# Kernel optimization log

Measured on AMD Instinct MI355X. Metric: run time of the kernel, lower is better.

Reference implementation:

```python
import jax, jax.numpy as jnp
import numpy as np

TOPK = 16          # static stand-in for dense_to_sparse(A_virtual): top-k neighbors per master node
LAMBDA_ATTN = 1.0  # VirtualGeneration temperature
GAMMA = 4.0        # gaussian radial basis width
R_CENTERS = 8      # radial_embedding.out_dim
NEG = -1e9


def _sh(v):
    # stand-in spherical harmonics: 16 monomials (lmax=3-ish) of the unit direction
    n = jnp.linalg.norm(v, axis=-1, keepdims=True)
    u = v / (n + 1e-9)
    x, y, z = u[:, 0], u[:, 1], u[:, 2]
    o = jnp.ones_like(x)
    return jnp.stack([o, x, y, z, x * x, y * y, z * z, x * y, x * z, y * z,
                      x * x * x, y * y * y, z * z * z, x * x * y, y * y * z, z * z * x], axis=-1)


def _radial(r):
    # gaussian radial basis, r: [E,1] -> [E,R]
    centers = jnp.linspace(0.0, 5.0, R_CENTERS, dtype=r.dtype)
    return jnp.exp(-GAMMA * (r - centers[None, :]) ** 2)


def _msgs(x, src, dst, sh, feats, Wr, wsh, n):
    # MACE-style conv message aggregation: radial-gated, SH-modulated gather/scatter
    gate = feats @ Wr                               # [E, Cin]
    msg = x[src] * gate * (sh @ wsh)[:, None]       # [E, Cin]
    return jax.ops.segment_sum(msg, dst, num_segments=n)


def _forward(h, pos, edge_index, edge_sh, edge_feats,
             W_loc_r, w_loc_sh, W_loc_out, W_prod_loc,
             W_ms1, b_ms1, W_ms2, b_ms2, Wq, Wk,
             W_a1, b_a1, W_a2, b_a2,
             W_h_r, w_h_sh, W_h_out, W_prod_h):
    N, D = h.shape
    D2 = W_loc_out.shape[1]
    S = W_ms1.shape[0]
    src, dst = edge_index[0], edge_index[1]

    # --- local conv + prod skip (h_local) ---
    h_up = _msgs(h, src, dst, edge_sh, edge_feats, W_loc_r, w_loc_sh, N) @ W_loc_out  # [N, D2]
    h_local = h_up @ W_prod_loc + jnp.pad(h, ((0, 0), (0, D2 - D)))
    h_scalar = h_local[:, :S]

    # --- master selection (MLP -> sigmoid -> hard threshold) ---
    m = jax.nn.sigmoid(jax.nn.relu(h_scalar @ W_ms1 + b_ms1) @ W_ms2 + b_ms2)[:, 0]
    mf = (m > 0.5).astype(h.dtype)

    # --- induced master-master edges: mask instead of dynamic subgraph extraction ---
    pair = mf[src] * mf[dst]
    vec_i = pos[src] - pos[dst]
    len_i = jnp.linalg.norm(vec_i, axis=-1, keepdims=True)
    sh_i = _sh(vec_i)
    rf_i = _radial(len_i) * pair[:, None]  # induced full_weights == 1, masked to master pairs

    # --- virtual edge generation: dense attention scores among masters, static top-k ---
    q = h_scalar @ Wq
    kk = h_scalar @ Wk
    scores_nn = (q @ kk.T) / (np.sqrt(S).astype(np.float32) * LAMBDA_ATTN)  # [N, N]
    pair_ok = (mf[:, None] * mf[None, :]) * (1.0 - jnp.eye(N, dtype=h.dtype))  # no self loops
    scores_nn = jnp.where(pair_ok > 0, scores_nn, NEG)
    topv, topi = jax.lax.top_k(scores_nn, TOPK)        # [N, K]
    vsrc = jnp.repeat(jnp.arange(N), TOPK)             # [N*K]
    vdst = topi.reshape(-1)
    vvalid = (topv.reshape(-1) > NEG / 2).astype(h.dtype)

    vec_v = pos[vsrc] - pos[vdst]
    len_v = jnp.linalg.norm(vec_v, axis=-1, keepdims=True)
    sh_v = _sh(vec_v)
    rf_v = _radial(len_v)

    # --- scatter-softmax attention over virtual edges (per destination) ---
    attn_in = jnp.concatenate([h_scalar[vsrc], h_scalar[vdst], rf_v], axis=-1)
    sc = (jax.nn.relu(attn_in @ W_a1 + b_a1) @ W_a2 + b_a2)[:, 0]
    sc = jnp.where(vvalid > 0, sc, NEG)
    mx = jax.ops.segment_max(sc, vdst, num_segments=N)
    ex = jnp.where(vvalid > 0, jnp.exp(sc - mx[vdst]), 0.0)
    den = jax.ops.segment_sum(ex, vdst, num_segments=N)
    wv = ex / (den[vdst] + 1e-12)
    rf_v = rf_v * wv[:, None]

    # --- hierarchical conv over induced + virtual master edges ---
    agg = (_msgs(h_local, src, dst, sh_i, rf_i, W_h_r, w_h_sh, N)
           + _msgs(h_local, vsrc, vdst, sh_v, rf_v, W_h_r, w_h_sh, N))
    h_m_up = agg @ W_h_out
    h_hier = (h_m_up @ W_prod_h + h_local) * mf[:, None]  # zero at non-master slots

    # --- gated combine ---
    return (1.0 - m)[:, None] * h_local + m[:, None] * h_hier


def setup_inputs():
    key = jax.random.key(0)
    ks = jax.random.split(key, 24)
    N, E, D, D2, S, R, L, HID = 4096, 131072, 128, 256, 128, 8, 16, 64

    def w(k, shape):
        return (jax.random.normal(k, shape, jnp.float32) / np.sqrt(shape[0]).astype(np.float32))

    return dict(
        h=jax.random.normal(ks[0], (N, D), jnp.float32),
        pos=jax.random.normal(ks[1], (N, 3), jnp.float32),
        edge_index=jax.random.randint(ks[2], (2, E), 0, N),
        edge_sh=jax.random.normal(ks[3], (E, L), jnp.float32),
        edge_feats=jax.random.normal(ks[4], (E, R), jnp.float32),
        batch=jnp.zeros((N,), jnp.int32),
        W_loc_r=w(ks[5], (R, D)),
        w_loc_sh=jax.random.normal(ks[6], (L,), jnp.float32) / 4.0,
        W_loc_out=w(ks[7], (D, D2)),
        W_prod_loc=w(ks[8], (D2, D2)),
        W_ms1=w(ks[9], (S, HID)), b_ms1=jnp.zeros((HID,), jnp.float32),
        W_ms2=w(ks[10], (HID, 1)), b_ms2=jnp.zeros((1,), jnp.float32),
        Wq=w(ks[11], (S, S)), Wk=w(ks[12], (S, S)),
        W_a1=w(ks[13], (2 * S + R, S)), b_a1=jnp.zeros((S,), jnp.float32),
        W_a2=w(ks[14], (S, 1)), b_a2=jnp.zeros((1,), jnp.float32),
        W_h_r=w(ks[15], (R, D2)),
        w_h_sh=jax.random.normal(ks[16], (L,), jnp.float32) / 4.0,
        W_h_out=w(ks[17], (D2, D2)),
        W_prod_h=w(ks[18], (D2, D2)),
    )


def reference(h, pos, edge_index, edge_sh, edge_feats, batch,
              W_loc_r, w_loc_sh, W_loc_out, W_prod_loc,
              W_ms1, b_ms1, W_ms2, b_ms2, Wq, Wk,
              W_a1, b_a1, W_a2, b_a2,
              W_h_r, w_h_sh, W_h_out, W_prod_h):
    # batch is unused by the original forward as well
    return _forward(h, pos, edge_index, edge_sh, edge_feats,
                    W_loc_r, w_loc_sh, W_loc_out, W_prod_loc,
                    W_ms1, b_ms1, W_ms2, b_ms2, Wq, Wk,
                    W_a1, b_a1, W_a2, b_a2,
                    W_h_r, w_h_sh, W_h_out, W_prod_h)
```

## Files before the change

kernel.cpp:

```cpp
#include <hip/hip_runtime.h>

typedef unsigned int u32;

#define NN 4096
#define EE 131072
#define DD 128
#define D2 256
#define SS 128
#define RR 8
#define LL 16
#define HH 64
#define TK 16
#define VSTRIDE 32
#define VV2 (NN*VSTRIDE)
#define NEGF -1000000000.0f
#define MNEGF -3.0e38f
#define SCLF 11.313708305358886719f
#define DELTA 1.0e-3f
#define CHUNK 1024
#define RCH 32
#define VCH 64
#define MAXCH_R 8192
#define MAXCH_V 5184

__device__ __forceinline__ float fadd(float a, float b) { return __fadd_rn(a, b); }
__device__ __forceinline__ float fsub(float a, float b) { return __fsub_rn(a, b); }
__device__ __forceinline__ float fmul(float a, float b) { return __fmul_rn(a, b); }
__device__ __forceinline__ float ffma(float a, float b, float c) { return __fmaf_rn(a, b, c); }

enum : size_t {
  B_CNTR   = 0,
  B_CNTV   = 16384,
  B_MXE    = 32768,
  ZERO_END = 49152,
  B_STARTR = 49152,
  B_STARTV = 69632,
  B_LISTR  = 90112,
  B_LISTV  = 614400,
  B_TOPI   = 1138688,
  B_WFAC   = 1662976,
  B_AMSG   = 2187264,
  B_HUP    = 4284416,
  B_HLOC   = 8478720,
  B_T1     = 12673024,
  B_MARR   = 13721600,
  B_MF     = 13737984,
  B_Q      = 13754368,
  B_KT     = 15851520,
  B_SC     = 17948672,
  B_WV     = 18472960,
  B_SUMR   = 18997248,
  B_SUMV   = 23191552,
  B_AGG    = 27385856,
  B_HMUP   = 31580160,
  B_CURR   = 35774464,
  B_CURV   = 35790848,
  B_P1     = 35807232,
  B_P2     = 37904384,
  B_TOTAL  = 40001536,
  B_ERP    = B_Q,
  B_EVP    = B_HUP,
  B_SHV1   = B_SUMR,
  B_SCHUNK = B_SUMR,
  B_CHT    = B_HUP + 3145728,
  O_CHJV   = 64,
  O_CHPV   = 64 + 4*MAXCH_V,
  O_CHJR   = 64 + 8*MAXCH_V,
  O_CHPR   = 64 + 8*MAXCH_V + 4*MAXCH_R,
  B_CHT2   = 40001536,
  B_SBIG   = 41943040,
  WS_BIG   = 109051904
};

__global__ void count_keys(const int* __restrict__ keys, int n, u32* __restrict__ cnt) {
  int e = blockIdx.x * 256 + threadIdx.x;
  if (e >= n) return;
  int d = keys[e];
  if (d >= 0) atomicAdd(&cnt[d], 1u);
}

__global__ __launch_bounds__(256) void scan_ex_par(const u32* __restrict__ cnt,
                                                   u32* __restrict__ start,
                                                   u32* __restrict__ cursor, int n,
                                                   int csz, u32* __restrict__ chCnt,
                                                   int* __restrict__ chJ,
                                                   int* __restrict__ chP) {
  __shared__ u32 part[256];
  __shared__ u32 cpart[256];
  int t = threadIdx.x;
  int per = n / 256;
  u32 s = 0;
  for (int i = 0; i < per; ++i) s += cnt[t*per + i];
  part[t] = s;
  __syncthreads();
  if (t == 0) {
    u32 run = 0;
    for (int i = 0; i < 256; ++i) { u32 v = part[i]; part[i] = run; run += v; }
    start[n] = run;
  }
  __syncthreads();
  u32 run = part[t];
  for (int i = 0; i < per; ++i) {
    int k = t*per + i;
    start[k] = run;
    cursor[k] = run;
    run += cnt[k];
  }
  if (csz > 0) {
    u32 cc = 0;
    for (int i = 0; i < per; ++i) {
      u32 len = cnt[t*per + i];
      cc += (len + (u32)csz - 1u) / (u32)csz;
    }
    cpart[t] = cc;
    __syncthreads();
    if (t == 0) {
      u32 r2 = 0;
      for (int i = 0; i < 256; ++i) { u32 v = cpart[i]; cpart[i] = r2; r2 += v; }
      *chCnt = r2;
    }
    __syncthreads();
    u32 b = cpart[t];
    u32 sb = part[t];
    for (int i = 0; i < per; ++i) {
      int k = t*per + i;
      u32 len = cnt[k];
      u32 nch = (len + (u32)csz - 1u) / (u32)csz;
      for (u32 kk = 0; kk < nch; ++kk) { chJ[b] = k; chP[b] = (int)(sb + kk*(u32)csz); ++b; }
      sb += len;
    }
  }
}

__global__ void fill_atomic(const int* __restrict__ keys, int n,
                            u32* __restrict__ cursor, int* __restrict__ list) {
  int e = blockIdx.x * 256 + threadIdx.x;
  if (e >= n) return;
  int d = keys[e];
  if (d < 0) return;
  u32 p = atomicAdd(&cursor[d], 1u);
  list[p] = e;
}

__global__ void build_chunks(const u32* __restrict__ start, int nseg, int csz,
                             u32* __restrict__ cnt, int* __restrict__ chJ,
                             int* __restrict__ chP) {
  int j = blockIdx.x * 256 + threadIdx.x;
  if (j >= nseg) return;
  u32 s0 = start[j], s1 = start[j + 1];
  if (s0 >= s1) return;
  int nch = (int)((s1 - s0) + (u32)csz - 1) / csz;
  u32 b = atomicAdd(cnt, (u32)nch);
  for (int k = 0; k < nch; ++k) {
    chJ[b + k] = j;
    chP[b + k] = (int)(s0 + (u32)k * (u32)csz);
  }
}

__global__ void edge_pre1(const float* __restrict__ esh, const float* __restrict__ wsh,
                          float* __restrict__ shv1) {
  int e = blockIdx.x * 256 + threadIdx.x;
  if (e >= EE) return;
  float s = 0.f;
  #pragma unroll
  for (int l = 0; l < LL; ++l) s = ffma(esh[e*LL + l], wsh[l], s);
  shv1[e] = s;
}

__global__ __launch_bounds__(128) void rep_msgs1(
    const float* __restrict__ h, const int* __restrict__ ei,
    const float* __restrict__ efeat,
    const float* __restrict__ Wr, const float* __restrict__ shv1,
    const u32* __restrict__ startR, const int* __restrict__ listR,
    float* __restrict__ amsg)
{
  __shared__ int   ssrc[64];
  __shared__ float sshv[64];
  __shared__ float sef[64][8];
  int d = blockIdx.x, c = threadIdx.x;
  float wr[RR];
  #pragma unroll
  for (int r = 0; r < RR; ++r) wr[r] = Wr[r*DD + c];
  float acc = 0.f;
  u32 s0 = startR[d], s1 = startR[d + 1];
  for (u32 t0 = s0; t0 < s1; t0 += 64) {
    int tl = (int)(s1 - t0 < 64u ? s1 - t0 : 64u);
    if (c < tl) {
      int e = listR[t0 + c];
      ssrc[c] = ei[e];
      sshv[c] = shv1[e];
      const float4* fe = reinterpret_cast<const float4*>(&efeat[(size_t)e*RR]);
      float4 f0 = fe[0], f1 = fe[1];
      sef[c][0]=f0.x; sef[c][1]=f0.y; sef[c][2]=f0.z; sef[c][3]=f0.w;
      sef[c][4]=f1.x; sef[c][5]=f1.y; sef[c][6]=f1.z; sef[c][7]=f1.w;
    }
    __syncthreads();
    int k = 0;
    for (; k + 4 <= tl; k += 4) {
      float h0 = h[(size_t)ssrc[k  ]*DD + c];
      float h1 = h[(size_t)ssrc[k+1]*DD + c];
      float h2 = h[(size_t)ssrc[k+2]*DD + c];
      float h3 = h[(size_t)ssrc[k+3]*DD + c];
      float g0 = 0.f, g1 = 0.f, g2 = 0.f, g3 = 0.f;
      #pragma unroll
      for (int r = 0; r < RR; ++r) {
        g0 = ffma(sef[k  ][r], wr[r], g0);
        g1 = ffma(sef[k+1][r], wr[r], g1);
        g2 = ffma(sef[k+2][r], wr[r], g2);
        g3 = ffma(sef[k+3][r], wr[r], g3);
      }
      acc = fadd(acc, fmul(fmul(h0, g0), sshv[k  ]));
      acc = fadd(acc, fmul(fmul(h1, g1), sshv[k+1]));
      acc = fadd(acc, fmul(fmul(h2, g2), sshv[k+2]));
      acc = fadd(acc, fmul(fmul(h3, g3), sshv[k+3]));
    }
    for (; k < tl; ++k) {
      float hv = h[(size_t)ssrc[k]*DD + c];
      float g = 0.f;
      #pragma unroll
      for (int r = 0; r < RR; ++r) g = ffma(sef[k][r], wr[r], g);
      acc = fadd(acc, fmul(fmul(hv, g), sshv[k]));
    }
    __syncthreads();
  }
  amsg[d*DD + c] = acc;
}

__global__ __launch_bounds__(256) void gemm64(
    const float* __restrict__ A, int lda,
    const float* __restrict__ B, int ldb,
    float* __restrict__ C, int ldc,
    int K, int mode,
    const float* __restrict__ x1,
    const float* __restrict__ marr, const float* __restrict__ mfarr,
    float* __restrict__ outp)
{
  __shared__ float As[16][68];
  __shared__ float Bs[16][68];
  int tid = threadIdx.x;
  int bm = blockIdx.x << 6, bn = blockIdx.y << 6;
  int tm = ((tid >> 4) << 2), tn = ((tid & 15) << 2);
  float acc[4][4] = {};
  for (int k0 = 0; k0 < K; k0 += 16) {
    #pragma unroll
    for (int t = 0; t < 4; ++t) {
      int idx = tid + (t << 8);
      int r = idx >> 4, c = idx & 15;
      As[c][r] = A[(size_t)(bm + r)*lda + k0 + c];
      int rb = idx >> 6, cb = idx & 63;
      Bs[rb][cb] = B[(size_t)(k0 + rb)*ldb + bn + cb];
    }
    __syncthreads();
    #pragma unroll
    for (int kk = 0; kk < 16; ++kk) {
      float4 av = *reinterpret_cast<const float4*>(&As[kk][tm]);
      float4 bv = *reinterpret_cast<const float4*>(&Bs[kk][tn]);
      float a0 = av.x, a1 = av.y, a2 = av.z, a3 = av.w;
      float b0 = bv.x, b1 = bv.y, b2 = bv.z, b3 = bv.w;
      acc[0][0]=ffma(a0,b0,acc[0][0]); acc[0][1]=ffma(a0,b1,acc[0][1]);
      acc[0][2]=ffma(a0,b2,acc[0][2]); acc[0][3]=ffma(a0,b3,acc[0][3]);
      acc[1][0]=ffma(a1,b0,acc[1][0]); acc[1][1]=ffma(a1,b1,acc[1][1]);
      acc[1][2]=ffma(a1,b2,acc[1][2]); acc[1][3]=ffma(a1,b3,acc[1][3]);
      acc[2][0]=ffma(a2,b0,acc[2][0]); acc[2][1]=ffma(a2,b1,acc[2][1]);
      acc[2][2]=ffma(a2,b2,acc[2][2]); acc[2][3]=ffma(a2,b3,acc[2][3]);
      acc[3][0]=ffma(a3,b0,acc[3][0]); acc[3][1]=ffma(a3,b1,acc[3][1]);
      acc[3][2]=ffma(a3,b2,acc[3][2]); acc[3][3]=ffma(a3,b3,acc[3][3]);
    }
    __syncthreads();
  }
  #pragma unroll
  for (int ii = 0; ii < 4; ++ii) {
    int r = bm + tm + ii;
    #pragma unroll
    for (int jj = 0; jj < 4; ++jj) {
      int c = bn + tn + jj;
      float v = acc[ii][jj];
      if (mode == 0) {
        C[(size_t)r*ldc + c] = v;
      } else if (mode == 1) {
        if (c < DD) v = fadd(v, x1[(size_t)r*DD + c]);
        C[(size_t)r*ldc + c] = v;
      } else if (mode == 2) {
        float hl = x1[(size_t)r*D2 + c];
        float hh = fmul(fadd(v, hl), mfarr[r]);
        float m = marr[r];
        outp[(size_t)r*D2 + c] = fadd(fmul(fsub(1.f, m), hl), fmul(m, hh));
      } else {
        C[(size_t)c*ldc + r] = v;
      }
    }
  }
}

__global__ __launch_bounds__(256, 2) void gemm_score128(
    const float* __restrict__ A, const float* __restrict__ B,
    const float* __restrict__ mf, int rowoff,
    float* __restrict__ S)
{
  __shared__ float As[16][68];
  __shared__ float Bs[16][136];
  int tid = threadIdx.x;
  int bm = blockIdx.x << 6;
  int bn = blockIdx.y << 7;
  int tm = ((tid >> 4) << 2), tn = ((tid & 15) << 2);
  float acc[4][8] = {};
  for (int k0 = 0; k0 < SS; k0 += 16) {
    {
      int row = tid >> 2, seg = tid & 3;
      const float4 av = *reinterpret_cast<const float4*>(
          &A[(size_t)(bm + row)*SS + k0 + (seg << 2)]);
      As[(seg<<2)+0][row] = av.x;
      As[(seg<<2)+1][row] = av.y;
      As[(seg<<2)+2][row] = av.z;
      As[(seg<<2)+3][row] = av.w;
    }
    #pragma unroll
    for (int t = 0; t < 2; ++t) {
      int f = tid + (t << 8);
      int rb = f >> 5, cb = (f & 31) << 2;
      const float4 bv = *reinterpret_cast<const float4*>(
          &B[(size_t)(k0 + rb)*NN + bn + cb]);
      *reinterpret_cast<float4*>(&Bs[rb][cb]) = bv;
    }
    __syncthreads();
    #pragma unroll
    for (int kk = 0; kk < 16; ++kk) {
      float4 av = *reinterpret_cast<const float4*>(&As[kk][tm]);
      float4 bl = *reinterpret_cast<const float4*>(&Bs[kk][tn]);
      float4 bh = *reinterpret_cast<const float4*>(&Bs[kk][tn + 64]);
      float a[4] = {av.x, av.y, av.z, av.w};
      float b[8] = {bl.x, bl.y, bl.z, bl.w, bh.x, bh.y, bh.z, bh.w};
      #pragma unroll
      for (int i = 0; i < 4; ++i)
        #pragma unroll
        for (int j = 0; j < 8; ++j)
          acc[i][j] = ffma(a[i], b[j], acc[i][j]);
    }
    __syncthreads();
  }
  #pragma unroll
  for (int ii = 0; ii < 4; ++ii) {
    int r = bm + tm + ii;
    int rg = rowoff + r;
    #pragma unroll
    for (int jj = 0; jj < 8; ++jj) {
      int c = bn + ((jj < 4) ? (tn + jj) : (tn + 64 + (jj - 4)));
      float s = __fdiv_rn(acc[ii][jj], SCLF);
      bool valid = (mf[c] > 0.5f) && (c != rg);
      S[(size_t)r*NN + c] = valid ? s : NEGF;
    }
  }
}

__global__ __launch_bounds__(256) void rep_sel(
    const float* __restrict__ S, int rowoff, const float* __restrict__ mf,
    int* __restrict__ topi, float* __restrict__ wfac)
{
  __shared__ float svals[4];
  __shared__ int   sidx[4];
  int tid = threadIdx.x;
  int row = rowoff + blockIdx.x;
  int base = row * VSTRIDE;
  if (mf[row] <= 0.5f) {
    if (tid < VSTRIDE) { topi[base + tid] = -1; wfac[base + tid] = 0.f; }
    return;
  }
  float4 vals[4];
  const float4* rp = reinterpret_cast<const float4*>(S + (size_t)blockIdx.x * NN);
  #pragma unroll
  for (int g = 0; g < 4; ++g) vals[g] = rp[tid + (g << 8)];
  int w = tid >> 6, lane = tid & 63;
  float v15 = 0.f, v16 = 0.f; int i15 = -1, i16 = -1;
  for (int it = 0; it < 17; ++it) {
    float bv = MNEGF; int bi = 1 << 30;
    #pragma unroll
    for (int g = 0; g < 4; ++g) {
      int j0 = (tid << 2) + (g << 10);
      { float v = vals[g].x; int j = j0;     if (v > bv || (v == bv && j < bi)) { bv = v; bi = j; } }
      { float v = vals[g].y; int j = j0 + 1; if (v > bv || (v == bv && j < bi)) { bv = v; bi = j; } }
      { float v = vals[g].z; int j = j0 + 2; if (v > bv || (v == bv && j < bi)) { bv = v; bi = j; } }
      { float v = vals[g].w; int j = j0 + 3; if (v > bv || (v == bv && j < bi)) { bv = v; bi = j; } }
    }
    #pragma unroll
    for (int off = 32; off > 0; off >>= 1) {
      float v2 = __shfl_down(bv, off);
      int j2 = __shfl_down(bi, off);
      if (v2 > bv || (v2 == bv && j2 < bi)) { bv = v2; bi = j2; }
    }
    if (lane == 0) { svals[w] = bv; sidx[w] = bi; }
    __syncthreads();
    float fv = svals[0]; int fi = sidx[0];
    #pragma unroll
    for (int k = 1; k < 4; ++k) {
      float v2 = svals[k]; int j2 = sidx[k];
      if (v2 > fv || (v2 == fv && j2 < fi)) { fv = v2; fi = j2; }
    }
    __syncthreads();
    #pragma unroll
    for (int g = 0; g < 4; ++g) {
      int j0 = (tid << 2) + (g << 10);
      if (fi == j0)     vals[g].x = MNEGF;
      if (fi == j0 + 1) vals[g].y = MNEGF;
      if (fi == j0 + 2) vals[g].z = MNEGF;
      if (fi == j0 + 3) vals[g].w = MNEGF;
    }
    if (it < 15) {
      if (tid == 0) {
        bool ok = fv > 0.5f * NEGF;
        topi[base + it] = ok ? fi : -1;
        wfac[base + it] = ok ? 1.f : 0.f;
      }
    } else if (it == 15) { v15 = fv; i15 = fi; }
    else                 { v16 = fv; i16 = fi; }
  }
  if (tid == 0) {
    bool b16 = v15 > 0.5f * NEGF;
    bool b17 = v16 > 0.5f * NEGF;
    bool contested = b16 && b17 && (fsub(v15, v16) < DELTA);
    topi[base + 15] = b16 ? i15 : -1;
    wfac[base + 15] = b16 ? (contested ? 0.5f : 1.f) : 0.f;
    topi[base + 16] = contested ? i16 : -1;
    wfac[base + 16] = contested ? 0.5f : 0.f;
  }
  if (tid >= 17 && tid < VSTRIDE) { topi[base + tid] = -1; wfac[base + tid] = 0.f; }
}

__global__ __launch_bounds__(64) void rep_mask(const float* __restrict__ t1,
    const float* __restrict__ b1, const float* __restrict__ W2,
    const float* __restrict__ b2, float* __restrict__ marr, float* __restrict__ mf)
{
  __shared__ float t3[HH];
  int n = blockIdx.x, hh = threadIdx.x;
  t3[hh] = fmaxf(fadd(t1[n*HH + hh], b1[hh]), 0.f);
  __syncthreads();
  if (hh == 0) {
    float acc = 0.f;
    for (int k = 0; k < HH; ++k) acc = ffma(t3[k], W2[k], acc);
    float z = fadd(acc, b2[0]);
    float m = __fdiv_rn(1.f, fadd(1.f, expf(-z)));
    marr[n] = m;
    mf[n] = (m > 0.5f) ? 1.f : 0.f;
  }
}

__device__ __forceinline__ float centerf(int r) {
  return (float)(((double)r * 5.0) / 7.0);
}

__global__ __launch_bounds__(256) void attn_edge2(
    const float* __restrict__ P1, const float* __restrict__ P2,
    const float* __restrict__ pos, const int* __restrict__ topi,
    const float* __restrict__ Wa1, const float* __restrict__ ba1,
    const float* __restrict__ Wa2, const float* __restrict__ ba2,
    float* __restrict__ sc, u32* __restrict__ mxe)
{
  __shared__ float wsum[4];
  __shared__ float srf[2][8];
  int tid = threadIdx.x;
  int eh = tid >> 7;
  int c = tid & 127;
  int idx = blockIdx.x * 2 + eh;
  int i = idx / 17;
  int k = idx - i * 17;
  int v = (i << 5) + k;
  int j = topi[v];
  if (c < 8 && j >= 0) {
    float vx = fsub(pos[i*3+0], pos[j*3+0]);
    float vy = fsub(pos[i*3+1], pos[j*3+1]);
    float vz = fsub(pos[i*3+2], pos[j*3+2]);
    float n2 = fadd(fadd(fmul(vx,vx), fmul(vy,vy)), fmul(vz,vz));
    float len = __fsqrt_rn(n2);
    float dr = fsub(len, centerf(c));
    srf[eh][c] = expf(fmul(-4.f, fmul(dr, dr)));
  }
  __syncthreads();
  float p = 0.f;
  if (j >= 0) {
    float t = fadd(P1[(size_t)i*SS + c], P2[(size_t)j*SS + c]);
    #pragma unroll
    for (int r = 0; r < RR; ++r) {
      t = ffma(srf[eh][r], Wa1[(256 + r)*SS + c], t);
    }
    t = fmaxf(fadd(t, ba1[c]), 0.f);
    p = fmul(t, Wa2[c]);
  }
  #pragma unroll
  for (int off = 32; off > 0; off >>= 1) p += __shfl_down(p, off);
  int wid = tid >> 6;
  if ((tid & 63) == 0) wsum[wid] = p;
  __syncthreads();
  if ((tid & 127) == 0 && j >= 0) {
    float acc = wsum[eh*2] + wsum[eh*2 + 1];
    float s = fadd(acc, ba2[0]);
    sc[v] = s;
    u32 u = __float_as_uint(s);
    u = (u & 0x80000000u) ? ~u : (u | 0x80000000u);
    atomicMax(&mxe[j], u);
  }
}

__global__ __launch_bounds__(64) void rep_denwv2(
    const float* __restrict__ sc, const u32* __restrict__ mxe,
    const u32* __restrict__ startV, const int* __restrict__ listV,
    const float* __restrict__ wfac, float* __restrict__ wvv)
{
  int j = blockIdx.x;
  int lane = threadIdx.x;
  u32 s0 = startV[j], s1 = startV[j + 1];
  if (s0 == s1) return;
  u32 ue = mxe[j];
  u32 b = (ue & 0x80000000u) ? (ue ^ 0x80000000u) : ~ue;
  float mx = __uint_as_float(b);
  float psum = 0.f;
  for (u32 idx = s0 + lane; idx < s1; idx += 64) {
    int v = listV[idx];
    float ex = fmul(wfac[v], expf(fsub(sc[v], mx)));
    wvv[v] = ex;
    psum += ex;
  }
  #pragma unroll
  for (int off = 32; off > 0; off >>= 1) psum += __shfl_down(psum, off);
  float den = __shfl(psum, 0);
  float dd = fadd(den, 1e-12f);
  for (u32 idx = s0 + lane; idx < s1; idx += 64) {
    int v = listV[idx];
    wvv[v] = __fdiv_rn(wvv[v], dd);
  }
}

__device__ __forceinline__ float shrep(float vx, float vy, float vz,
                                       const float* __restrict__ w) {
  float n2 = fadd(fadd(fmul(vx,vx), fmul(vy,vy)), fmul(vz,vz));
  float n = __fsqrt_rn(n2);
  float dnm = fadd(n, 1e-9f);
  float x = __fdiv_rn(vx, dnm), y = __fdiv_rn(vy, dnm), z = __fdiv_rn(vz, dnm);
  float t[16];
  t[0]=1.f; t[1]=x; t[2]=y; t[3]=z;
  t[4]=fmul(x,x); t[5]=fmul(y,y); t[6]=fmul(z,z);
  t[7]=fmul(x,y); t[8]=fmul(x,z); t[9]=fmul(y,z);
  t[10]=fmul(fmul(x,x),x); t[11]=fmul(fmul(y,y),y); t[12]=fmul(fmul(z,z),z);
  t[13]=fmul(fmul(x,x),y); t[14]=fmul(fmul(y,y),z); t[15]=fmul(fmul(z,z),x);
  float s = 0.f;
  #pragma unroll
  for (int l = 0; l < 16; ++l) s = ffma(t[l], w[l], s);
  return s;
}

__global__ void edge_pre_rv(const float* __restrict__ pos, const int* __restrict__ ei,
                            const float* __restrict__ mf, const float* __restrict__ whsh,
                            const int* __restrict__ listR, float* __restrict__ erp,
                            const int* __restrict__ topi, const float* __restrict__ wvv,
                            const u32* __restrict__ startV, const int* __restrict__ listV,
                            float* __restrict__ evp) {
  int b = blockIdx.x;
  if (b < EE/256) {
    int p = b * 256 + threadIdx.x;
    int e = listR[p];
    int src = ei[e], dst = ei[EE + e];
    float* op = erp + (size_t)p * 9;
    if (mf[src] <= 0.5f || mf[dst] <= 0.5f) {
      #pragma unroll
      for (int r = 0; r < 9; ++r) op[r] = 0.f;
      return;
    }
    float vx = fsub(pos[src*3+0], pos[dst*3+0]);
    float vy = fsub(pos[src*3+1], pos[dst*3+1]);
    float vz = fsub(pos[src*3+2], pos[dst*3+2]);
    op[0] = shrep(vx, vy, vz, whsh);
    float len = __fsqrt_rn(fadd(fadd(fmul(vx,vx), fmul(vy,vy)), fmul(vz,vz)));
    #pragma unroll
    for (int r = 0; r < RR; ++r) {
      float dr = fsub(len, centerf(r));
      op[1 + r] = expf(fmul(-4.f, fmul(dr, dr)));
    }
  } else {
    int p = (b - EE/256) * 256 + threadIdx.x;
    if (p >= (int)startV[NN]) return;
    int v = listV[p];
    int i = v >> 5;
    int j = topi[v];
    float w = wvv[v];
    float* op = evp + (size_t)p * 9;
    float vx = fsub(pos[i*3+0], pos[j*3+0]);
    float vy = fsub(pos[i*3+1], pos[j*3+1]);
    float vz = fsub(pos[i*3+2], pos[j*3+2]);
    op[0] = shrep(vx, vy, vz, whsh);
    float len = __fsqrt_rn(fadd(fadd(fmul(vx,vx), fmul(vy,vy)), fmul(vz,vz)));
    #pragma unroll
    for (int r = 0; r < RR; ++r) {
      float dr = fsub(len, centerf(r));
      op[1 + r] = fmul(expf(fmul(-4.f, fmul(dr, dr))), w);
    }
  }
}

__global__ __launch_bounds__(256) void rep_msgs2r4(
    const float* __restrict__ hloc, const int* __restrict__ ei,
    const float* __restrict__ Whr, const float* __restrict__ erp,
    const u32* __restrict__ startR, const int* __restrict__ listR,
    const u32* __restrict__ cnt, const int* __restrict__ chJ,
    const int* __restrict__ chP, float* __restrict__ sumR)
{
  __shared__ int   ssrc[RCH];
  __shared__ float sep[RCH][9];
  int b = blockIdx.x;
  if (b >= (int)(*cnt)) return;
  int d = chJ[b], c = threadIdx.x;
  u32 p0 = (u32)chP[b];
  u32 p1 = startR[d + 1];
  u32 pe = p0 + RCH; if (pe < p1) p1 = pe;
  int len = (int)(p1 - p0);
  if (c < len) ssrc[c] = ei[listR[p0 + c]];
  for (int t = c; t < len*9; t += 256) (&sep[0][0])[t] = erp[(size_t)p0*9 + t];
  __syncthreads();
  float whr[RR];
  #pragma unroll
  for (int r = 0; r < RR; ++r) whr[r] = Whr[r*D2 + c];
  float acc = 0.f;
  int k = 0;
  for (; k + 4 <= len; k += 4) {
    float h0 = hloc[(size_t)ssrc[k  ]*D2 + c];
    float h1 = hloc[(size_t)ssrc[k+1]*D2 + c];
    float h2 = hloc[(size_t)ssrc[k+2]*D2 + c];
    float h3 = hloc[(size_t)ssrc[k+3]*D2 + c];
    float g0 = 0.f, g1 = 0.f, g2 = 0.f, g3 = 0.f;
    #pragma unroll
    for (int r = 0; r < RR; ++r) {
      g0 = ffma(sep[k  ][1 + r], whr[r], g0);
      g1 = ffma(sep[k+1][1 + r], whr[r], g1);
      g2 = ffma(sep[k+2][1 + r], whr[r], g2);
      g3 = ffma(sep[k+3][1 + r], whr[r], g3);
    }
    acc = fadd(acc, fmul(fmul(h0, g0), sep[k  ][0]));
    acc = fadd(acc, fmul(fmul(h1, g1), sep[k+1][0]));
    acc = fadd(acc, fmul(fmul(h2, g2), sep[k+2][0]));
    acc = fadd(acc, fmul(fmul(h3, g3), sep[k+3][0]));
  }
  for (; k < len; ++k) {
    float hv = hloc[(size_t)ssrc[k]*D2 + c];
    float g = 0.f;
    #pragma unroll
    for (int r = 0; r < RR; ++r) g = ffma(sep[k][1 + r], whr[r], g);
    acc = fadd(acc, fmul(fmul(hv, g), sep[k][0]));
  }
  atomicAdd(&sumR[(size_t)d*D2 + c], acc);
}

__global__ __launch_bounds__(256) void rep_msgs2v4(
    const float* __restrict__ hloc, const int* __restrict__ listV,
    const float* __restrict__ Whr, const float* __restrict__ evp,
    const u32* __restrict__ startV,
    const u32* __restrict__ cnt, const int* __restrict__ chJ,
    const int* __restrict__ chP, float* __restrict__ sumR)
{
  __shared__ int   si[VCH];
  __shared__ float sep[VCH][9];
  int b = blockIdx.x;
  if (b >= (int)(*cnt)) return;
  int j = chJ[b], c = threadIdx.x;
  u32 p0 = (u32)chP[b];
  u32 p1 = startV[j + 1];
  u32 pe = p0 + VCH; if (pe < p1) p1 = pe;
  int len = (int)(p1 - p0);
  if (c < len) si[c] = listV[p0 + c] >> 5;
  for (int t = c; t < len*9; t += 256) (&sep[0][0])[t] = evp[(size_t)p0*9 + t];
  __syncthreads();
  float whr[RR];
  #pragma unroll
  for (int r = 0; r < RR; ++r) whr[r] = Whr[r*D2 + c];
  float acc = 0.f;
  int k = 0;
  for (; k + 4 <= len; k += 4) {
    float h0 = hloc[(size_t)si[k  ]*D2 + c];
    float h1 = hloc[(size_t)si[k+1]*D2 + c];
    float h2 = hloc[(size_t)si[k+2]*D2 + c];
    float h3 = hloc[(size_t)si[k+3]*D2 + c];
    float g0 = 0.f, g1 = 0.f, g2 = 0.f, g3 = 0.f;
    #pragma unroll
    for (int r = 0; r < RR; ++r) {
      g0 = ffma(sep[k  ][1 + r], whr[r], g0);
      g1 = ffma(sep[k+1][1 + r], whr[r], g1);
      g2 = ffma(sep[k+2][1 + r], whr[r], g2);
      g3 = ffma(sep[k+3][1 + r], whr[r], g3);
    }
    acc = fadd(acc, fmul(fmul(h0, g0), sep[k  ][0]));
    acc = fadd(acc, fmul(fmul(h1, g1), sep[k+1][0]));
    acc = fadd(acc, fmul(fmul(h2, g2), sep[k+2][0]));
    acc = fadd(acc, fmul(fmul(h3, g3), sep[k+3][0]));
  }
  for (; k < len; ++k) {
    float hv = hloc[(size_t)si[k]*D2 + c];
    float g = 0.f;
    #pragma unroll
    for (int r = 0; r < RR; ++r) g = ffma(sep[k][1 + r], whr[r], g);
    acc = fadd(acc, fmul(fmul(hv, g), sep[k][0]));
  }
  atomicAdd(&sumR[(size_t)j*D2 + c], acc);
}

extern "C" void kernel_launch(void* const* d_in, const int* in_sizes, int n_in,
                              void* d_out, int out_size, void* d_ws, size_t ws_size,
                              hipStream_t stream)
{
  char* wsb = (char*)d_ws;
  const float* h     = (const float*)d_in[0];
  const float* pos   = (const float*)d_in[1];
  const int*   ei    = (const int*)d_in[2];
  const float* esh   = (const float*)d_in[3];
  const float* efeat = (const float*)d_in[4];
  const float* Wlr   = (const float*)d_in[6];
  const float* wlsh  = (const float*)d_in[7];
  const float* Wlo   = (const float*)d_in[8];
  const float* Wpl   = (const float*)d_in[9];
  const float* Wms1  = (const float*)d_in[10];
  const float* bms1  = (const float*)d_in[11];
  const float* Wms2  = (const float*)d_in[12];
  const float* bms2  = (const float*)d_in[13];
  const float* Wq    = (const float*)d_in[14];
  const float* Wk    = (const float*)d_in[15];
  const float* Wa1   = (const float*)d_in[16];
  const float* ba1   = (const float*)d_in[17];
  const float* Wa2   = (const float*)d_in[18];
  const float* ba2   = (const float*)d_in[19];
  const float* Whr   = (const float*)d_in[20];
  const float* whsh  = (const float*)d_in[21];
  const float* Who   = (const float*)d_in[22];
  const float* Wph   = (const float*)d_in[23];

  u32* cntR   = (u32*)(wsb + B_CNTR);
  u32* cntV   = (u32*)(wsb + B_CNTV);
  u32* mxe    = (u32*)(wsb + B_MXE);
  u32* startR = (u32*)(wsb + B_STARTR);
  u32* startV = (u32*)(wsb + B_STARTV);
  u32* curR   = (u32*)(wsb + B_CURR);
  u32* curV   = (u32*)(wsb + B_CURV);
  int* listR  = (int*)(wsb + B_LISTR);
  int* listV  = (int*)(wsb + B_LISTV);
  int* topi   = (int*)(wsb + B_TOPI);
  float* wfac = (float*)(wsb + B_WFAC);
  float* amsg = (float*)(wsb + B_AMSG);
  float* hup  = (float*)(wsb + B_HUP);
  float* hloc = (float*)(wsb + B_HLOC);
  float* t1   = (float*)(wsb + B_T1);
  float* marr = (float*)(wsb + B_MARR);
  float* mf   = (float*)(wsb + B_MF);
  float* q    = (float*)(wsb + B_Q);
  float* kT   = (float*)(wsb + B_KT);
  float* sc   = (float*)(wsb + B_SC);
  float* wvv  = (float*)(wsb + B_WV);
  float* sumR = (float*)(wsb + B_SUMR);
  float* hmup = (float*)(wsb + B_HMUP);
  float* P1   = (float*)(wsb + B_P1);
  float* P2   = (float*)(wsb + B_P2);
  float* erp  = (float*)(wsb + B_ERP);
  float* evp  = (float*)(wsb + B_EVP);
  float* shv1 = (float*)(wsb + B_SHV1);

  const bool big = ws_size >= (size_t)WS_BIG;
  char* cht = wsb + (big ? B_CHT2 : B_CHT);
  u32* chCntV = (u32*)(cht);
  u32* chCntR = (u32*)(cht + 4);
  int* chJv   = (int*)(cht + O_CHJV);
  int* chPv   = (int*)(cht + O_CHPV);
  int* chJr   = (int*)(cht + O_CHJR);
  int* chPr   = (int*)(cht + O_CHPR);
  float* Sbuf = (float*)(wsb + (big ? B_SBIG : B_SCHUNK));

  hipMemsetAsync(d_ws, 0, ZERO_END, stream);

  count_keys<<<EE/256, 256, 0, stream>>>(ei + EE, EE, cntR);
  if (big)
    scan_ex_par<<<1, 256, 0, stream>>>(cntR, startR, curR, NN, RCH, chCntR, chJr, chPr);
  else
    scan_ex_par<<<1, 256, 0, stream>>>(cntR, startR, curR, NN, 0, nullptr, nullptr, nullptr);
  fill_atomic<<<EE/256, 256, 0, stream>>>(ei + EE, EE, curR, listR);

  edge_pre1<<<EE/256, 256, 0, stream>>>(esh, wlsh, shv1);
  rep_msgs1<<<NN, 128, 0, stream>>>(h, ei, efeat, Wlr, shv1, startR, listR, amsg);
  gemm64<<<dim3(64,4), 256, 0, stream>>>(amsg, DD, Wlo, D2, hup, D2, DD, 0,
                                         nullptr, nullptr, nullptr, nullptr);
  gemm64<<<dim3(64,4), 256, 0, stream>>>(hup, D2, Wpl, D2, hloc, D2, D2, 1,
                                         h, nullptr, nullptr, nullptr);
  gemm64<<<dim3(64,1), 256, 0, stream>>>(hloc, D2, Wms1, HH, t1, HH, SS, 0,
                                         nullptr, nullptr, nullptr, nullptr);
  rep_mask<<<NN, 64, 0, stream>>>(t1, bms1, Wms2, bms2, marr, mf);
  gemm64<<<dim3(64,2), 256, 0, stream>>>(hloc, D2, Wq, SS, q, SS, SS, 0,
                                         nullptr, nullptr, nullptr, nullptr);
  gemm64<<<dim3(64,2), 256, 0, stream>>>(hloc, D2, Wk, SS, kT, NN, SS, 3,
                                         nullptr, nullptr, nullptr, nullptr);

  if (big) {
    gemm_score128<<<dim3(NN/64, NN/128), 256, 0, stream>>>(q, kT, mf, 0, Sbuf);
    rep_sel<<<NN, 256, 0, stream>>>(Sbuf, 0, mf, topi, wfac);
  } else {
    for (int c0 = 0; c0 < NN; c0 += CHUNK) {
      gemm_score128<<<dim3(CHUNK/64, NN/128), 256, 0, stream>>>(q + (size_t)c0*SS, kT,
                                                                mf, c0, Sbuf);
      rep_sel<<<CHUNK, 256, 0, stream>>>(Sbuf, c0, mf, topi, wfac);
    }
  }

  hipMemsetAsync(wsb + B_SUMR, 0, 4194304, stream);

  count_keys<<<VV2/256, 256, 0, stream>>>(topi, VV2, cntV);
  if (big)
    scan_ex_par<<<1, 256, 0, stream>>>(cntV, startV, curV, NN, VCH, chCntV, chJv, chPv);
  else
    scan_ex_par<<<1, 256, 0, stream>>>(cntV, startV, curV, NN, 0, nullptr, nullptr, nullptr);
  fill_atomic<<<VV2/256, 256, 0, stream>>>(topi, VV2, curV, listV);

  gemm64<<<dim3(64,2), 256, 0, stream>>>(hloc, D2, Wa1, SS, P1, SS, SS, 0,
                                         nullptr, nullptr, nullptr, nullptr);
  gemm64<<<dim3(64,2), 256, 0, stream>>>(hloc, D2, Wa1 + 128*SS, SS, P2, SS, SS, 0,
                                         nullptr, nullptr, nullptr, nullptr);
  attn_edge2<<<(NN*17)/2, 256, 0, stream>>>(P1, P2, pos, topi, Wa1, ba1, Wa2, ba2,
                                            sc, mxe);
  rep_denwv2<<<NN, 64, 0, stream>>>(sc, mxe, startV, listV, wfac, wvv);

  if (!big) {
    hipMemsetAsync(cht, 0, 8, stream);
    build_chunks<<<NN/256, 256, 0, stream>>>(startV, NN, VCH, chCntV, chJv, chPv);
    build_chunks<<<NN/256, 256, 0, stream>>>(startR, NN, RCH, chCntR, chJr, chPr);
  }

  edge_pre_rv<<<EE/256 + (NN*17 + 255)/256, 256, 0, stream>>>(
      pos, ei, mf, whsh, listR, erp, topi, wvv, startV, listV, evp);

  rep_msgs2r4<<<MAXCH_R, 256, 0, stream>>>(hloc, ei, Whr, erp, startR, listR,
                                           chCntR, chJr, chPr, sumR);
  rep_msgs2v4<<<MAXCH_V, 256, 0, stream>>>(hloc, listV, Whr, evp, startV,
                                           chCntV, chJv, chPv, sumR);

  gemm64<<<dim3(64,4), 256, 0, stream>>>(sumR, D2, Who, D2, hmup, D2, D2, 0,
                                         nullptr, nullptr, nullptr, nullptr);
  gemm64<<<dim3(64,4), 256, 0, stream>>>(hmup, D2, Wph, D2, nullptr, D2, D2, 2,
                                         hloc, marr, mf, (float*)d_out);
}
```

Before: 527.4 us.

## Pack value and index into 64-bit keys for incremental top-k selection

Rewrites the per-row top-17 selection to encode each score and its index into one order-preserving 64-bit key. Each thread keeps a cached local max and each wavefront keeps a cached wave max. Per iteration, only the wavefront holding the winner rescans and re-reduces, so the full 16-element scan and shuffle reduction no longer run every iteration in every wave. Double-buffered shared slots drop one barrier per iteration. The cost is 64-bit compares and shuffles and more registers, which may lower occupancy.

```diff
diff --git a/kernel.cpp b/kernel.cpp
--- a/kernel.cpp
+++ b/kernel.cpp
@@ -1,6 +1,7 @@
 #include <hip/hip_runtime.h>
 
 typedef unsigned int u32;
+typedef unsigned long long u64;
 
 #define NN 4096
 #define EE 131072
@@ -352,12 +353,25 @@
   }
 }
 
+__device__ __forceinline__ u64 enc_key(float v, int j) {
+  u32 u = __float_as_uint(v);
+  u = (u & 0x80000000u) ? ~u : (u | 0x80000000u);
+  return ((u64)u << 32) | (u32)(0xFFFFFFFFu - (u32)j);
+}
+__device__ __forceinline__ float dec_val(u64 k) {
+  u32 e = (u32)(k >> 32);
+  u32 u = (e & 0x80000000u) ? (e ^ 0x80000000u) : ~e;
+  return __uint_as_float(u);
+}
+__device__ __forceinline__ int dec_idx(u64 k) {
+  return (int)(0xFFFFFFFFu - (u32)k);
+}
+
 __global__ __launch_bounds__(256) void rep_sel(
     const float* __restrict__ S, int rowoff, const float* __restrict__ mf,
     int* __restrict__ topi, float* __restrict__ wfac)
 {
-  __shared__ float svals[4];
-  __shared__ int   sidx[4];
+  __shared__ u64 wm[2][4];
   int tid = threadIdx.x;
   int row = rowoff + blockIdx.x;
   int base = row * VSTRIDE;
@@ -365,53 +379,66 @@
     if (tid < VSTRIDE) { topi[base + tid] = -1; wfac[base + tid] = 0.f; }
     return;
   }
-  float4 vals[4];
+  u64 kk[16];
   const float4* rp = reinterpret_cast<const float4*>(S + (size_t)blockIdx.x * NN);
   #pragma unroll
-  for (int g = 0; g < 4; ++g) vals[g] = rp[tid + (g << 8)];
-  int w = tid >> 6, lane = tid & 63;
+  for (int g = 0; g < 4; ++g) {
+    float4 v = rp[tid + (g << 8)];
+    int j0 = (tid << 2) + (g << 10);
+    kk[4*g+0] = enc_key(v.x, j0);
+    kk[4*g+1] = enc_key(v.y, j0 + 1);
+    kk[4*g+2] = enc_key(v.z, j0 + 2);
+    kk[4*g+3] = enc_key(v.w, j0 + 3);
+  }
+  u64 cmx = 0;
+  #pragma unroll
+  for (int i = 0; i < 16; ++i) cmx = (kk[i] > cmx) ? kk[i] : cmx;
+  int w = tid >> 6;
+  u64 rv = cmx;
+  #pragma unroll
+  for (int off = 32; off > 0; off >>= 1) {
+    u64 o = __shfl_down(rv, off);
+    if (o > rv) rv = o;
+  }
+  rv = __shfl(rv, 0);
+
   float v15 = 0.f, v16 = 0.f; int i15 = -1, i16 = -1;
   for (int it = 0; it < 17; ++it) {
-    float bv = MNEGF; int bi = 1 << 30;
-    #pragma unroll
-    for (int g = 0; g < 4; ++g) {
-      int j0 = (tid << 2) + (g << 10);
-      { float v = vals[g].x; int j = j0;     if (v > bv || (v == bv && j < bi)) { bv = v; bi = j; } }
-      { float v = vals[g].y; int j = j0 + 1; if (v > bv || (v == bv && j < bi)) { bv = v; bi = j; } }
-      { float v = vals[g].z; int j = j0 + 2; if (v > bv || (v == bv && j < bi)) { bv = v; bi = j; } }
-      { float v = vals[g].w; int j = j0 + 3; if (v > bv || (v == bv && j < bi)) { bv = v; bi = j; } }
-    }
-    #pragma unroll
-    for (int off = 32; off > 0; off >>= 1) {
-      float v2 = __shfl_down(bv, off);
-      int j2 = __shfl_down(bi, off);
-      if (v2 > bv || (v2 == bv && j2 < bi)) { bv = v2; bi = j2; }
-    }
-    if (lane == 0) { svals[w] = bv; sidx[w] = bi; }
+    int p = it & 1;
+    if ((tid & 63) == 0) wm[p][w] = rv;
     __syncthreads();
-    float fv = svals[0]; int fi = sidx[0];
-    #pragma unroll
-    for (int k = 1; k < 4; ++k) {
-      float v2 = svals[k]; int j2 = sidx[k];
-      if (v2 > fv || (v2 == fv && j2 < fi)) { fv = v2; fi = j2; }
-    }
-    __syncthreads();
-    #pragma unroll
-    for (int g = 0; g < 4; ++g) {
-      int j0 = (tid << 2) + (g << 10);
-      if (fi == j0)     vals[g].x = MNEGF;
-      if (fi == j0 + 1) vals[g].y = MNEGF;
-      if (fi == j0 + 2) vals[g].z = MNEGF;
-      if (fi == j0 + 3) vals[g].w = MNEGF;
-    }
-    if (it < 15) {
-      if (tid == 0) {
+    u64 m0 = wm[p][0], m1 = wm[p][1], m2 = wm[p][2], m3 = wm[p][3];
+    u64 g01 = (m0 > m1) ? m0 : m1;
+    u64 g23 = (m2 > m3) ? m2 : m3;
+    u64 gmax = (g01 > g23) ? g01 : g23;
+    if (tid == 0) {
+      float fv = dec_val(gmax);
+      int fi = dec_idx(gmax);
+      if (it < 15) {
         bool ok = fv > 0.5f * NEGF;
         topi[base + it] = ok ? fi : -1;
         wfac[base + it] = ok ? 1.f : 0.f;
+      } else if (it == 15) { v15 = fv; i15 = fi; }
+      else                 { v16 = fv; i16 = fi; }
+    }
+    if (rv == gmax) {
+      if (cmx == gmax) {
+        u64 nm = 0;
+        #pragma unroll
+        for (int i = 0; i < 16; ++i) {
+          kk[i] = (kk[i] == gmax) ? 0ull : kk[i];
+          nm = (kk[i] > nm) ? kk[i] : nm;
+        }
+        cmx = nm;
       }
-    } else if (it == 15) { v15 = fv; i15 = fi; }
-    else                 { v16 = fv; i16 = fi; }
+      u64 r2 = cmx;
+      #pragma unroll
+      for (int off = 32; off > 0; off >>= 1) {
+        u64 o = __shfl_down(r2, off);
+        if (o > r2) r2 = o;
+      }
+      rv = __shfl(r2, 0);
+    }
   }
   if (tid == 0) {
     bool b16 = v15 > 0.5f * NEGF;
```

New measurement: 514.5 us. 2.4% less time.
